# Optimization experiments

Hardware: AMD Instinct MI355X
Metric: run time of the kernel (lower is better)

The kernel has to match this reference:

```python
import jax, jax.numpy as jnp
import numpy as np

D_MODEL = 2048
H_TOTAL = 32
D_HEAD = D_MODEL // H_TOTAL  # 64
H_ACTIVE = 4
ROPE_BASE = 10000.0


def _apply_rope(t, cos, sin):
    # t: [B, H, T, DH]; cos/sin: [T, DH//2]; interleaved pair rotation
    t1 = t[..., 0::2]
    t2 = t[..., 1::2]
    r1 = t1 * cos - t2 * sin
    r2 = t1 * sin + t2 * cos
    return jnp.stack([r1, r2], axis=-1).reshape(t.shape)


def setup_inputs() -> dict:
    key = jax.random.key(0)
    ks = jax.random.split(key, 4)
    x = jax.random.normal(ks[0], (4, 1024, D_MODEL), dtype=jnp.float32)
    w_router = jax.random.normal(ks[1], (D_MODEL, H_TOTAL), dtype=jnp.float32) * 0.02
    w_qkv = jax.random.normal(ks[2], (D_MODEL, 3 * D_MODEL), dtype=jnp.float32) * 0.02
    w_out = jax.random.normal(ks[3], (D_MODEL, D_MODEL), dtype=jnp.float32) * 0.02
    return {"x": x, "w_router": w_router, "w_qkv": w_qkv, "w_out": w_out}


def reference(x, w_router, w_qkv, w_out):
    B, T, _ = x.shape
    # --- SwitchRouter: per-token probabilities over heads ---
    probs = jax.nn.softmax(x @ w_router, axis=-1)            # [B, T, H]
    # top-h_active heads per token (dense-math equivalent of sparse dispatch)
    _, top_idx = jax.lax.top_k(probs, H_ACTIVE)              # [B, T, HA]
    mask = jnp.sum(jax.nn.one_hot(top_idx, H_TOTAL, dtype=x.dtype), axis=-2)  # [B, T, H]
    gate = probs * mask                                      # router-scored gate

    # --- QKV projection ---
    qkv = x @ w_qkv                                          # [B, T, 3D]
    q, k, v = jnp.split(qkv, 3, axis=-1)
    def to_heads(t):
        return t.reshape(B, T, H_TOTAL, D_HEAD).transpose(0, 2, 1, 3)  # [B, H, T, DH]
    q, k, v = to_heads(q), to_heads(k), to_heads(v)

    # --- RoPE ---
    inv_freq = 1.0 / (ROPE_BASE ** (jnp.arange(0, D_HEAD, 2, dtype=jnp.float32) / D_HEAD))
    ang = jnp.arange(T, dtype=jnp.float32)[:, None] * inv_freq[None, :]  # [T, DH/2]
    cos, sin = jnp.cos(ang), jnp.sin(ang)
    q = _apply_rope(q, cos, sin)
    k = _apply_rope(k, cos, sin)

    # --- causal SDPA ---
    scores = jnp.einsum('bhqd,bhkd->bhqk', q, k) / np.float32(np.sqrt(D_HEAD))
    causal = jnp.tril(jnp.ones((T, T), dtype=bool))
    scores = jnp.where(causal, scores, jnp.finfo(scores.dtype).min)
    attn = jax.nn.softmax(scores, axis=-1)
    out = jnp.einsum('bhqk,bhkd->bhqd', attn, v)             # [B, H, T, DH]

    # --- gate: only active heads contribute (scatter-back equivalent) ---
    out = out * gate.transpose(0, 2, 1)[..., None]           # [B, H, T, DH]
    out = out.transpose(0, 2, 1, 3).reshape(B, T, D_MODEL)
    return out @ w_out
```

## Files before the change

### kernel.cpp

```cpp
#include <hip/hip_runtime.h>
#include <hip/hip_bf16.h>
#include <stdint.h>
#include <stddef.h>

typedef __attribute__((ext_vector_type(8))) short bf16x8;
typedef __attribute__((ext_vector_type(8))) unsigned short u16x8;
typedef __attribute__((ext_vector_type(4))) float f32x4;
typedef __attribute__((ext_vector_type(16))) float f32x16;

#define TT 1024

__device__ __forceinline__ unsigned short f2bf(float f){
  unsigned u = __builtin_bit_cast(unsigned, f);
  unsigned r = 0x7fffu + ((u >> 16) & 1u);
  return (unsigned short)((u + r) >> 16);
}
__device__ __forceinline__ float bf2f(unsigned short s){
  unsigned u = ((unsigned)s) << 16;
  return __builtin_bit_cast(float, u);
}
__device__ __forceinline__ void gload16(const unsigned short* g, unsigned short* l){
  __builtin_amdgcn_global_load_lds(
      (const __attribute__((address_space(1))) void*)g,
      (__attribute__((address_space(3))) void*)l, 16, 0, 0);
}

#define MFMA32(a, b, c) __builtin_amdgcn_mfma_f32_32x32x16_bf16((a), (b), (c), 0, 0, 0)
#define MFMA_B16(a, b, c) __builtin_amdgcn_mfma_f32_16x16x32_bf16((a), (b), (c), 0, 0, 0)

__global__ void transpose_cast_kernel(const float* __restrict__ in, unsigned short* __restrict__ out,
                                      int R, int C){
  __shared__ float tile[32][33];
  int c0 = blockIdx.x * 32, r0 = blockIdx.y * 32;
  for (int i = threadIdx.y; i < 32; i += 8)
    tile[i][threadIdx.x] = in[(size_t)(r0 + i) * C + c0 + threadIdx.x];
  __syncthreads();
  for (int i = threadIdx.y; i < 32; i += 8)
    out[(size_t)(c0 + i) * R + r0 + threadIdx.x] = f2bf(tile[threadIdx.x][i]);
}

__global__ void rope_table_kernel(float* __restrict__ tab){
  int idx = blockIdx.x * 256 + threadIdx.x;
  int pos = idx >> 5, i = idx & 31;
  float freq = powf(10000.0f, -(float)i / 32.0f);
  float ang = (float)pos * freq;
  tab[idx * 2]     = cosf(ang);
  tab[idx * 2 + 1] = sinf(ang);
}

__global__ __launch_bounds__(256) void prep_kernel(const float* __restrict__ x,
                                                   const float* __restrict__ wr,
                                                   unsigned short* __restrict__ x_bf,
                                                   float* __restrict__ gate,
                                                   unsigned char* __restrict__ heads4){
  __shared__ float xc[8 * 256];
  __shared__ float red[8 * 8 * 32];
  const int tid = threadIdx.x;
  const int tok0 = blockIdx.x * 8;
  const int p = tid >> 5, h = tid & 31;
  float acc[8] = {0.f,0.f,0.f,0.f,0.f,0.f,0.f,0.f};

  for (int kb = 0; kb < 8; kb++){
    __syncthreads();
    {
      int tok = tid >> 5, e = (tid & 31) * 8;
      const float* xp = x + (size_t)(tok0 + tok) * 2048 + kb * 256 + e;
      float4 v0 = *(const float4*)xp, v1 = *(const float4*)(xp + 4);
      float vals[8] = {v0.x, v0.y, v0.z, v0.w, v1.x, v1.y, v1.z, v1.w};
      u16x8 ob;
      #pragma unroll
      for (int jj = 0; jj < 8; jj++) ob[jj] = f2bf(vals[jj]);
      *(u16x8*)(x_bf + (size_t)(tok0 + tok) * 2048 + kb * 256 + e) = ob;
      #pragma unroll
      for (int jj = 0; jj < 8; jj++) xc[tok * 256 + e + jj] = vals[jj];
    }
    __syncthreads();
    const float* wp = wr + (size_t)(kb * 256 + p * 32) * 32 + h;
    #pragma unroll 4
    for (int j = 0; j < 32; j++){
      float wv = wp[j * 32];
      #pragma unroll
      for (int tok = 0; tok < 8; tok++)
        acc[tok] += xc[tok * 256 + p * 32 + j] * wv;
    }
  }
  #pragma unroll
  for (int tok = 0; tok < 8; tok++) red[(p * 8 + tok) * 32 + h] = acc[tok];
  __syncthreads();
  {
    int lane = tid & 63;
    int tok = (tid >> 6) * 2 + (lane >> 5);
    int hh = lane & 31;
    float logit = 0.f;
    #pragma unroll
    for (int pp = 0; pp < 8; pp++) logit += red[(pp * 8 + tok) * 32 + hh];
    float m = logit;
    #pragma unroll
    for (int s = 16; s >= 1; s >>= 1) m = fmaxf(m, __shfl_xor(m, s));
    float e = __expf(logit - m);
    float sum = e;
    #pragma unroll
    for (int s = 16; s >= 1; s >>= 1) sum += __shfl_xor(sum, s);
    float prob = e / sum;
    float v = logit; int sel = 0;
    #pragma unroll
    for (int rr2 = 0; rr2 < 4; rr2++){
      float bv = v; int bi = hh;
      #pragma unroll
      for (int s = 16; s >= 1; s >>= 1){
        float ov = __shfl_xor(bv, s); int oi = __shfl_xor(bi, s);
        if (ov > bv || (ov == bv && oi < bi)) { bv = ov; bi = oi; }
      }
      if (hh == bi) { sel = 1; v = -3.4e38f; }
    }
    gate[(size_t)(tok0 + tok) * 32 + hh] = sel ? prob : 0.f;
    unsigned long long bal = __ballot(sel != 0);
    unsigned selmask = (unsigned)(bal >> ((lane >> 5) * 32));
    if (sel){
      int r = __popc(selmask & ((1u << hh) - 1u));
      heads4[(size_t)(tok0 + tok) * 4 + r] = (unsigned char)hh;
    }
  }
}

__global__ void compact_kernel(const unsigned char* __restrict__ heads4,
                               unsigned short* __restrict__ idx, int* __restrict__ counts){
  int bh = blockIdx.x;
  int b = bh >> 5, h = bh & 31;
  int lane = threadIdx.x;
  int base = 0;
  for (int c = 0; c < 16; c++){
    int t = c * 64 + lane;
    unsigned u = ((const unsigned*)heads4)[b * 1024 + t];
    int r = -1;
    if (((u      ) & 255) == (unsigned)h) r = 0;
    else if (((u >>  8) & 255) == (unsigned)h) r = 1;
    else if (((u >> 16) & 255) == (unsigned)h) r = 2;
    else if (((u >> 24) & 255) == (unsigned)h) r = 3;
    bool act = (r >= 0);
    unsigned long long mask = __ballot(act);
    int pos = base + __popcll(mask & ((1ull << lane) - 1ull));
    if (act) idx[bh * 1024 + pos] = (unsigned short)(t | (r << 10));
    base += __popcll(mask);
  }
  if (lane == 0) counts[bh] = base;
}

__global__ __launch_bounds__(256) void qgemm_kernel(const unsigned short* __restrict__ x_bf,
                                                    const unsigned short* __restrict__ wqkvT,
                                                    const unsigned short* __restrict__ idx,
                                                    const int* __restrict__ counts,
                                                    const float* __restrict__ tab,
                                                    unsigned short* __restrict__ qact){
  __shared__ float red[4][64][64];
  const int bh = blockIdx.x, qt = blockIdx.y;
  const int count = counts[bh];
  if (qt * 64 >= count) return;
  const int b = bh >> 5, h = bh & 31;
  const int tid = threadIdx.x, lane = tid & 63, w = tid >> 6;
  const int li = lane & 15, lg = lane >> 4;
  const int nvalid = min(64, count - qt * 64);
  const unsigned short* myidx = idx + bh * 1024 + qt * 64;

  int atok[4];
  #pragma unroll
  for (int ai = 0; ai < 4; ai++){
    int s = ai * 16 + li;
    atok[ai] = (s < nvalid) ? (myidx[s] & 1023) : 0;
  }
  const unsigned short* Bbase = wqkvT + (size_t)(h * 64) * 2048;

  f32x4 acc[4][4];
  #pragma unroll
  for (int i = 0; i < 4; i++)
    #pragma unroll
    for (int j = 0; j < 4; j++) acc[i][j] = f32x4{0.f, 0.f, 0.f, 0.f};

  const int k0w = w * 512;
  #pragma unroll 2
  for (int ks = 0; ks < 16; ks++){
    int k0 = k0w + ks * 32 + lg * 8;
    bf16x8 af[4], bw[4];
    #pragma unroll
    for (int ai = 0; ai < 4; ai++)
      af[ai] = *(const bf16x8*)(x_bf + (size_t)(b * 1024 + atok[ai]) * 2048 + k0);
    #pragma unroll
    for (int ni = 0; ni < 4; ni++)
      bw[ni] = *(const bf16x8*)(Bbase + (size_t)(ni * 16 + li) * 2048 + k0);
    #pragma unroll
    for (int ai = 0; ai < 4; ai++)
      #pragma unroll
      for (int ni = 0; ni < 4; ni++)
        acc[ai][ni] = MFMA_B16(af[ai], bw[ni], acc[ai][ni]);
  }
  #pragma unroll
  for (int ai = 0; ai < 4; ai++)
    #pragma unroll
    for (int ni = 0; ni < 4; ni++)
      #pragma unroll
      for (int rr = 0; rr < 4; rr++)
        red[w][ai * 16 + lg * 4 + rr][ni * 16 + li] = acc[ai][ni][rr];
  __syncthreads();

  int q = tid >> 2, dbase = (tid & 3) * 16;
  if (q < nvalid){
    int e = myidx[q];
    int tok = e & 1023, r = e >> 10;
    unsigned short* op = qact + ((size_t)((b << 10) + tok) * 4 + r) * 64;
    const float* tp = tab + ((size_t)tok * 32 + (dbase >> 1)) * 2;
    #pragma unroll
    for (int p = 0; p < 8; p++){
      int d0 = dbase + 2 * p;
      float v0 = red[0][q][d0] + red[1][q][d0] + red[2][q][d0] + red[3][q][d0];
      float v1 = red[0][q][d0 + 1] + red[1][q][d0 + 1] + red[2][q][d0 + 1] + red[3][q][d0 + 1];
      float c = tp[2 * p], s = tp[2 * p + 1];
      op[d0]     = f2bf(v0 * c - v1 * s);
      op[d0 + 1] = f2bf(v0 * s + v1 * c);
    }
  }
}

template<int EPI>
__global__ __launch_bounds__(256, 1) void gemm32(const unsigned short* __restrict__ A,
                                                 const unsigned short* __restrict__ Bt,
                                                 float* __restrict__ Cf,
                                                 unsigned short* __restrict__ kbuf,
                                                 unsigned short* __restrict__ vt,
                                                 const float* __restrict__ tab,
                                                 int N, int K, int nbm){
  extern __shared__ unsigned short smem[];
  const int nblk = gridDim.x;
  const int raw = blockIdx.x;
  const int tile = (raw & 7) * (nblk >> 3) + (raw >> 3);
  const int bn = tile / nbm, bm = tile % nbm;

  const int tid = threadIdx.x, lane = tid & 63, wid = tid >> 6;
  const int wrow = wid >> 1, wcol = wid & 1;
  const int l31 = lane & 31, hi = lane >> 5;
  const int X = (l31 & 7) << 4;

  const unsigned short* gA[8];
  const unsigned short* gB[4];
  #pragma unroll
  for (int p = 0; p < 8; p++){
    int L = tid * 16 + p * 4096;
    int r = L >> 7, c = (L & 127) ^ ((r & 7) << 4);
    gA[p] = A + (size_t)(bm * 256 + r) * K + (c >> 1);
  }
  #pragma unroll
  for (int p = 0; p < 4; p++){
    int L = tid * 16 + p * 4096;
    int r = L >> 7, c = (L & 127) ^ ((r & 7) << 4);
    gB[p] = Bt + (size_t)(bn * 128 + r) * K + (c >> 1);
  }

  auto stageA0 = [&](int tt){
    unsigned short* b = smem + (tt % 3) * 24576;
    size_t ko = (size_t)tt * 64;
    gload16(gA[0] + ko, b + tid * 8);
    gload16(gA[1] + ko, b + tid * 8 + 2048);
    gload16(gA[2] + ko, b + tid * 8 + 4096);
    gload16(gA[3] + ko, b + tid * 8 + 6144);
  };
  auto stageA1 = [&](int tt){
    unsigned short* b = smem + (tt % 3) * 24576;
    size_t ko = (size_t)tt * 64;
    gload16(gA[4] + ko, b + tid * 8 + 8192);
    gload16(gA[5] + ko, b + tid * 8 + 10240);
    gload16(gA[6] + ko, b + tid * 8 + 12288);
    gload16(gA[7] + ko, b + tid * 8 + 14336);
  };
  auto stageB = [&](int tt){
    unsigned short* b = smem + (tt % 3) * 24576 + 16384;
    size_t ko = (size_t)tt * 64;
    gload16(gB[0] + ko, b + tid * 8);
    gload16(gB[1] + ko, b + tid * 8 + 2048);
    gload16(gB[2] + ko, b + tid * 8 + 4096);
    gload16(gB[3] + ko, b + tid * 8 + 6144);
  };

  f32x16 acc[4][2];
  #pragma unroll
  for (int i = 0; i < 4; i++)
    #pragma unroll
    for (int j = 0; j < 2; j++) acc[i][j] = f32x16{0,0,0,0,0,0,0,0,0,0,0,0,0,0,0,0};

  const int NT = K >> 6;
  stageA0(0); stageA1(0); stageB(0);
  stageA0(1); stageA1(1); stageB(1);

  const int arow = (wrow * 128 + l31) * 64;
  const int brow = 16384 + (wcol * 64 + l31) * 64;

  for (int t = 0; t < NT; ++t){
    if (t < NT - 1) asm volatile("s_waitcnt vmcnt(12)" ::: "memory");
    else            asm volatile("s_waitcnt vmcnt(0)" ::: "memory");
    __builtin_amdgcn_s_barrier();
    __builtin_amdgcn_sched_barrier(0);
    const unsigned short* bs = smem + (t % 3) * 24576;
    const bool st = (t + 2 < NT);
    #pragma unroll
    for (int ks = 0; ks < 4; ks++){
      const int kp = ((ks * 32 + hi * 16) ^ X) >> 1;
      bf16x8 a0 = *(const bf16x8*)(bs + arow +        kp);
      bf16x8 a1 = *(const bf16x8*)(bs + arow + 2048 + kp);
      bf16x8 a2 = *(const bf16x8*)(bs + arow + 4096 + kp);
      bf16x8 a3 = *(const bf16x8*)(bs + arow + 6144 + kp);
      bf16x8 b0 = *(const bf16x8*)(bs + brow +        kp);
      bf16x8 b1 = *(const bf16x8*)(bs + brow + 2048 + kp);
      if (st && ks == 0) stageA0(t + 2);
      if (st && ks == 1) stageA1(t + 2);
      if (st && ks == 2) stageB(t + 2);
      acc[0][0] = MFMA32(a0, b0, acc[0][0]); acc[0][1] = MFMA32(a0, b1, acc[0][1]);
      acc[1][0] = MFMA32(a1, b0, acc[1][0]); acc[1][1] = MFMA32(a1, b1, acc[1][1]);
      acc[2][0] = MFMA32(a2, b0, acc[2][0]); acc[2][1] = MFMA32(a2, b1, acc[2][1]);
      acc[3][0] = MFMA32(a3, b0, acc[3][0]); acc[3][1] = MFMA32(a3, b1, acc[3][1]);
    }
  }

  if (EPI == 1){
    if (bn < 16){
      #pragma unroll
      for (int i = 0; i < 4; i++){
        #pragma unroll
        for (int j = 0; j < 2; j++){
          int col = bn * 128 + wcol * 64 + j * 32 + l31;
          int ii = (col & 63) >> 1;
          #pragma unroll
          for (int g = 0; g < 4; g++){
            #pragma unroll
            for (int rr = 0; rr < 4; rr++){
              int row = bm * 256 + wrow * 128 + i * 32 + g * 8 + hi * 4 + rr;
              int pos = row & (TT - 1);
              const float* tp = tab + ((size_t)pos * 32 + ii) * 2;
              float c = tp[0], s = tp[1];
              float val = acc[i][j][g * 4 + rr];
              float pv = __shfl_xor(val, 1);
              float res = (lane & 1) ? (pv * s + val * c) : (val * c - pv * s);
              kbuf[(size_t)row * 2048 + col] = f2bf(res);
            }
          }
        }
      }
    } else {
      #pragma unroll
      for (int i = 0; i < 4; i++){
        #pragma unroll
        for (int j = 0; j < 2; j++){
          int vcol = bn * 128 + wcol * 64 + j * 32 + l31 - 2048;
          int hh = vcol >> 6, d = vcol & 63;
          int row0 = bm * 256 + wrow * 128 + i * 32 + hi * 4;
          int b = row0 >> 10, t0 = row0 & (TT - 1);
          #pragma unroll
          for (int g = 0; g < 4; g++){
            ushort4 pk;
            pk.x = f2bf(acc[i][j][g * 4 + 0]); pk.y = f2bf(acc[i][j][g * 4 + 1]);
            pk.z = f2bf(acc[i][j][g * 4 + 2]); pk.w = f2bf(acc[i][j][g * 4 + 3]);
            *(ushort4*)(vt + ((size_t)((b * 32 + hh) * 64 + d)) * TT + t0 + g * 8) = pk;
          }
        }
      }
    }
  } else {
    #pragma unroll
    for (int i = 0; i < 4; i++){
      #pragma unroll
      for (int j = 0; j < 2; j++){
        int col = bn * 128 + wcol * 64 + j * 32 + l31;
        #pragma unroll
        for (int g = 0; g < 4; g++){
          #pragma unroll
          for (int rr = 0; rr < 4; rr++){
            size_t row = (size_t)(bm * 256 + wrow * 128 + i * 32 + g * 8 + hi * 4 + rr);
            Cf[row * N + col] = acc[i][j][g * 4 + rr];
          }
        }
      }
    }
  }
}

__global__ __launch_bounds__(256) void attn_sparse_kernel(const unsigned short* __restrict__ qact,
                                                          const unsigned short* __restrict__ kbuf,
                                                          const unsigned short* __restrict__ vt,
                                                          const float* __restrict__ gate,
                                                          const unsigned short* __restrict__ idx,
                                                          const int* __restrict__ counts,
                                                          unsigned short* __restrict__ attn_out){
  __shared__ unsigned short Ks[64 * 64];
  __shared__ unsigned short Vs[64 * 64];
  __shared__ unsigned short Ps[4][16 * 64];
  const int bh = blockIdx.x, qt = blockIdx.y;
  const int count = counts[bh];
  if (qt * 64 >= count) return;
  const int b = bh >> 5, h = bh & 31;
  const int tid = threadIdx.x, lane = tid & 63, w = tid >> 6;
  const int li = lane & 15, lg = lane >> 4;
  const unsigned short* myidx = idx + bh * 1024 + qt * 64;
  const int nvalid = min(64, count - qt * 64);
  const int qmax = myidx[nvalid - 1] & 1023;

  int qi[4];
  #pragma unroll
  for (int r = 0; r < 4; r++){
    int s = w * 16 + lg * 4 + r;
    qi[r] = (s < nvalid) ? (myidx[s] & 1023) : -1;
  }
  bf16x8 qf0, qf1;
  {
    int s = w * 16 + li;
    int e2 = (s < nvalid) ? myidx[s] : 0;
    const unsigned short* qp = qact + ((size_t)((b << 10) + (e2 & 1023)) * 4 + (e2 >> 10)) * 64;
    qf0 = *(const bf16x8*)(qp + lg * 8);
    qf1 = *(const bf16x8*)(qp + 32 + lg * 8);
  }
  f32x4 o[4];
  #pragma unroll
  for (int i = 0; i < 4; i++) o[i] = f32x4{0.f, 0.f, 0.f, 0.f};
  float m_run[4], l_run[4];
  #pragma unroll
  for (int r = 0; r < 4; r++){ m_run[r] = -1e30f; l_run[r] = 0.f; }

  const int nkt = (qmax >> 6) + 1;
  for (int kt = 0; kt < nkt; kt++){
    const int kb = kt * 64;
    #pragma unroll
    for (int s2 = 0; s2 < 2; s2++){
      int s = s2 * 256 + tid;
      int r = s >> 3, c = (s & 7) * 8;
      gload16(kbuf + (size_t)(b * TT + kb + r) * 2048 + h * 64 + c, &Ks[s * 8]);
      gload16(vt + (size_t)(bh * 64 + r) * TT + kb + c, &Vs[s * 8]);
    }
    __syncthreads();

    f32x4 s4[4];
    #pragma unroll
    for (int ni = 0; ni < 4; ni++){
      bf16x8 k0 = *(const bf16x8*)(&Ks[(ni * 16 + li) * 64 + lg * 8]);
      bf16x8 k1 = *(const bf16x8*)(&Ks[(ni * 16 + li) * 64 + 32 + lg * 8]);
      f32x4 t = f32x4{0.f, 0.f, 0.f, 0.f};
      t = MFMA_B16(qf0, k0, t);
      t = MFMA_B16(qf1, k1, t);
      s4[ni] = t;
    }
    float mt[4];
    #pragma unroll
    for (int r = 0; r < 4; r++) mt[r] = -1e30f;
    #pragma unroll
    for (int ni = 0; ni < 4; ni++){
      int kidx = kb + ni * 16 + li;
      #pragma unroll
      for (int r = 0; r < 4; r++){
        float val = s4[ni][r] * 0.125f;
        val = (kidx <= qi[r]) ? val : -1e30f;
        s4[ni][r] = val;
        mt[r] = fmaxf(mt[r], val);
      }
    }
    #pragma unroll
    for (int r = 0; r < 4; r++){
      #pragma unroll
      for (int sh = 8; sh >= 1; sh >>= 1) mt[r] = fmaxf(mt[r], __shfl_xor(mt[r], sh));
      float mnew = fmaxf(m_run[r], mt[r]);
      float corr = __expf(m_run[r] - mnew);
      m_run[r] = mnew;
      l_run[r] *= corr;
      #pragma unroll
      for (int j = 0; j < 4; j++) o[j][r] *= corr;
    }
    float rs[4] = {0.f, 0.f, 0.f, 0.f};
    #pragma unroll
    for (int ni = 0; ni < 4; ni++)
      #pragma unroll
      for (int r = 0; r < 4; r++){
        float p = __expf(s4[ni][r] - m_run[r]);
        s4[ni][r] = p;
        rs[r] += p;
      }
    #pragma unroll
    for (int r = 0; r < 4; r++){
      #pragma unroll
      for (int sh = 8; sh >= 1; sh >>= 1) rs[r] += __shfl_xor(rs[r], sh);
      l_run[r] += rs[r];
    }
    #pragma unroll
    for (int ni = 0; ni < 4; ni++)
      #pragma unroll
      for (int r = 0; r < 4; r++)
        Ps[w][(lg * 4 + r) * 64 + ni * 16 + li] = f2bf(s4[ni][r]);
    #pragma unroll
    for (int ks = 0; ks < 2; ks++){
      bf16x8 pa = *(const bf16x8*)(&Ps[w][li * 64 + ks * 32 + lg * 8]);
      #pragma unroll
      for (int ni = 0; ni < 4; ni++){
        bf16x8 vb = *(const bf16x8*)(&Vs[(ni * 16 + li) * 64 + ks * 32 + lg * 8]);
        o[ni] = MFMA_B16(pa, vb, o[ni]);
      }
    }
    __syncthreads();
  }
  #pragma unroll
  for (int r = 0; r < 4; r++){
    if (qi[r] < 0) continue;
    float g = gate[(size_t)(b * TT + qi[r]) * 32 + h];
    float inv = g / l_run[r];
    #pragma unroll
    for (int ni = 0; ni < 4; ni++)
      attn_out[(size_t)(b * TT + qi[r]) * 2048 + h * 64 + ni * 16 + li] = f2bf(o[ni][r] * inv);
  }
}

extern "C" void kernel_launch(void* const* d_in, const int* in_sizes, int n_in,
                              void* d_out, int out_size, void* d_ws, size_t ws_size,
                              hipStream_t stream){
  const float* x        = (const float*)d_in[0];
  const float* w_router = (const float*)d_in[1];
  const float* w_qkv    = (const float*)d_in[2];
  const float* w_out    = (const float*)d_in[3];
  float* out = (float*)d_out;
  char* ws = (char*)d_ws;

  unsigned short* kbuf   = (unsigned short*)(ws);
  unsigned short* vt     = (unsigned short*)(ws + 16777216);
  unsigned short* qact   = (unsigned short*)(ws + 33554432);
  unsigned short* idx    = (unsigned short*)(ws + 37748736);
  int* counts            = (int*)(ws + 38010880);
  unsigned char* heads4  = (unsigned char*)(ws + 38011392);
  unsigned short* x_bf   = (unsigned short*)(ws + 50331648);
  unsigned short* wqkvT  = (unsigned short*)(ws + 67108864);
  unsigned short* woutT  = (unsigned short*)(ws + 92274688);
  float* gate            = (float*)(ws + 100663296);
  float* tab             = (float*)(ws + 101187584);
  unsigned short* attn   = x_bf;

  constexpr int GEMM_LDS = 147456;
  (void)hipFuncSetAttribute(reinterpret_cast<const void*>(&gemm32<1>),
                            hipFuncAttributeMaxDynamicSharedMemorySize, GEMM_LDS);
  (void)hipFuncSetAttribute(reinterpret_cast<const void*>(&gemm32<0>),
                            hipFuncAttributeMaxDynamicSharedMemorySize, GEMM_LDS);

  hipLaunchKernelGGL(transpose_cast_kernel, dim3(192, 64), dim3(32, 8), 0, stream, w_qkv, wqkvT, 2048, 6144);
  hipLaunchKernelGGL(transpose_cast_kernel, dim3(64, 64), dim3(32, 8), 0, stream, w_out, woutT, 2048, 2048);
  hipLaunchKernelGGL(rope_table_kernel, dim3(128), dim3(256), 0, stream, tab);
  hipLaunchKernelGGL(prep_kernel, dim3(512), dim3(256), 0, stream, x, w_router, x_bf, gate, heads4);
  hipLaunchKernelGGL(compact_kernel, dim3(128), dim3(64), 0, stream, heads4, idx, counts);
  hipLaunchKernelGGL((gemm32<1>), dim3(512), dim3(256), GEMM_LDS, stream,
                     x_bf, wqkvT + (size_t)2048 * 2048, (float*)nullptr, kbuf, vt, tab, 4096, 2048, 16);
  hipLaunchKernelGGL(qgemm_kernel, dim3(128, 16), dim3(256), 0, stream,
                     x_bf, wqkvT, idx, counts, tab, qact);
  (void)hipMemsetAsync(attn, 0, (size_t)4096 * 2048 * 2, stream);
  hipLaunchKernelGGL(attn_sparse_kernel, dim3(128, 16), dim3(256), 0, stream,
                     qact, kbuf, vt, gate, idx, counts, attn);
  hipLaunchKernelGGL((gemm32<0>), dim3(256), dim3(256), GEMM_LDS, stream,
                     attn, woutT, out, (unsigned short*)nullptr, (unsigned short*)nullptr,
                     (const float*)nullptr, 2048, 2048, 16);
}
```

Measured before the change: 263.5 us.

## Fuse Q projection into attention, retile GEMMs, merge prep kernels, swizzle LDS

```diff
diff --git a/kernel.cpp b/kernel.cpp
--- a/kernel.cpp
+++ b/kernel.cpp
@@ -28,10 +28,15 @@
 #define MFMA32(a, b, c) __builtin_amdgcn_mfma_f32_32x32x16_bf16((a), (b), (c), 0, 0, 0)
 #define MFMA_B16(a, b, c) __builtin_amdgcn_mfma_f32_16x16x32_bf16((a), (b), (c), 0, 0, 0)
 
-__global__ void transpose_cast_kernel(const float* __restrict__ in, unsigned short* __restrict__ out,
-                                      int R, int C){
+__global__ void transpose_w_kernel(const float* __restrict__ wqkv, const float* __restrict__ wout,
+                                   unsigned short* __restrict__ wqkvT, unsigned short* __restrict__ woutT){
   __shared__ float tile[32][33];
-  int c0 = blockIdx.x * 32, r0 = blockIdx.y * 32;
+  const float* in; unsigned short* out; int C;
+  int bx = blockIdx.x;
+  if (bx < 192){ in = wqkv; out = wqkvT; C = 6144; }
+  else         { in = wout; out = woutT; C = 2048; bx -= 192; }
+  const int R = 2048;
+  int c0 = bx * 32, r0 = blockIdx.y * 32;
   for (int i = threadIdx.y; i < 32; i += 8)
     tile[i][threadIdx.x] = in[(size_t)(r0 + i) * C + c0 + threadIdx.x];
   __syncthreads();
@@ -39,27 +44,28 @@
     out[(size_t)(c0 + i) * R + r0 + threadIdx.x] = f2bf(tile[threadIdx.x][i]);
 }
 
-__global__ void rope_table_kernel(float* __restrict__ tab){
-  int idx = blockIdx.x * 256 + threadIdx.x;
-  int pos = idx >> 5, i = idx & 31;
-  float freq = powf(10000.0f, -(float)i / 32.0f);
-  float ang = (float)pos * freq;
-  tab[idx * 2]     = cosf(ang);
-  tab[idx * 2 + 1] = sinf(ang);
-}
-
 __global__ __launch_bounds__(256) void prep_kernel(const float* __restrict__ x,
                                                    const float* __restrict__ wr,
                                                    unsigned short* __restrict__ x_bf,
                                                    float* __restrict__ gate,
-                                                   unsigned char* __restrict__ heads4){
+                                                   unsigned char* __restrict__ heads4,
+                                                   float* __restrict__ tab){
   __shared__ float xc[8 * 256];
   __shared__ float red[8 * 8 * 32];
   const int tid = threadIdx.x;
   const int tok0 = blockIdx.x * 8;
   const int p = tid >> 5, h = tid & 31;
+
+  if (blockIdx.x < 128){
+    int i2 = blockIdx.x * 256 + tid;
+    int pos = i2 >> 5, ii = i2 & 31;
+    float freq = powf(10000.0f, -(float)ii / 32.0f);
+    float ang = (float)pos * freq;
+    tab[i2 * 2]     = cosf(ang);
+    tab[i2 * 2 + 1] = sinf(ang);
+  }
+
   float acc[8] = {0.f,0.f,0.f,0.f,0.f,0.f,0.f,0.f};
-
   for (int kb = 0; kb < 8; kb++){
     __syncthreads();
     {
@@ -146,89 +152,18 @@
   if (lane == 0) counts[bh] = base;
 }
 
-__global__ __launch_bounds__(256) void qgemm_kernel(const unsigned short* __restrict__ x_bf,
-                                                    const unsigned short* __restrict__ wqkvT,
-                                                    const unsigned short* __restrict__ idx,
-                                                    const int* __restrict__ counts,
-                                                    const float* __restrict__ tab,
-                                                    unsigned short* __restrict__ qact){
-  __shared__ float red[4][64][64];
-  const int bh = blockIdx.x, qt = blockIdx.y;
-  const int count = counts[bh];
-  if (qt * 64 >= count) return;
-  const int b = bh >> 5, h = bh & 31;
-  const int tid = threadIdx.x, lane = tid & 63, w = tid >> 6;
-  const int li = lane & 15, lg = lane >> 4;
-  const int nvalid = min(64, count - qt * 64);
-  const unsigned short* myidx = idx + bh * 1024 + qt * 64;
-
-  int atok[4];
-  #pragma unroll
-  for (int ai = 0; ai < 4; ai++){
-    int s = ai * 16 + li;
-    atok[ai] = (s < nvalid) ? (myidx[s] & 1023) : 0;
-  }
-  const unsigned short* Bbase = wqkvT + (size_t)(h * 64) * 2048;
-
-  f32x4 acc[4][4];
-  #pragma unroll
-  for (int i = 0; i < 4; i++)
-    #pragma unroll
-    for (int j = 0; j < 4; j++) acc[i][j] = f32x4{0.f, 0.f, 0.f, 0.f};
-
-  const int k0w = w * 512;
-  #pragma unroll 2
-  for (int ks = 0; ks < 16; ks++){
-    int k0 = k0w + ks * 32 + lg * 8;
-    bf16x8 af[4], bw[4];
-    #pragma unroll
-    for (int ai = 0; ai < 4; ai++)
-      af[ai] = *(const bf16x8*)(x_bf + (size_t)(b * 1024 + atok[ai]) * 2048 + k0);
-    #pragma unroll
-    for (int ni = 0; ni < 4; ni++)
-      bw[ni] = *(const bf16x8*)(Bbase + (size_t)(ni * 16 + li) * 2048 + k0);
-    #pragma unroll
-    for (int ai = 0; ai < 4; ai++)
-      #pragma unroll
-      for (int ni = 0; ni < 4; ni++)
-        acc[ai][ni] = MFMA_B16(af[ai], bw[ni], acc[ai][ni]);
-  }
-  #pragma unroll
-  for (int ai = 0; ai < 4; ai++)
-    #pragma unroll
-    for (int ni = 0; ni < 4; ni++)
-      #pragma unroll
-      for (int rr = 0; rr < 4; rr++)
-        red[w][ai * 16 + lg * 4 + rr][ni * 16 + li] = acc[ai][ni][rr];
-  __syncthreads();
-
-  int q = tid >> 2, dbase = (tid & 3) * 16;
-  if (q < nvalid){
-    int e = myidx[q];
-    int tok = e & 1023, r = e >> 10;
-    unsigned short* op = qact + ((size_t)((b << 10) + tok) * 4 + r) * 64;
-    const float* tp = tab + ((size_t)tok * 32 + (dbase >> 1)) * 2;
-    #pragma unroll
-    for (int p = 0; p < 8; p++){
-      int d0 = dbase + 2 * p;
-      float v0 = red[0][q][d0] + red[1][q][d0] + red[2][q][d0] + red[3][q][d0];
-      float v1 = red[0][q][d0 + 1] + red[1][q][d0 + 1] + red[2][q][d0 + 1] + red[3][q][d0 + 1];
-      float c = tp[2 * p], s = tp[2 * p + 1];
-      op[d0]     = f2bf(v0 * c - v1 * s);
-      op[d0 + 1] = f2bf(v0 * s + v1 * c);
-    }
-  }
-}
-
-template<int EPI>
-__global__ __launch_bounds__(256, 1) void gemm32(const unsigned short* __restrict__ A,
-                                                 const unsigned short* __restrict__ Bt,
-                                                 float* __restrict__ Cf,
-                                                 unsigned short* __restrict__ kbuf,
-                                                 unsigned short* __restrict__ vt,
-                                                 const float* __restrict__ tab,
-                                                 int N, int K, int nbm){
+template<int MREP, int EPI>
+__global__ __launch_bounds__(256, 2) void gemmk(const unsigned short* __restrict__ A,
+                                                const unsigned short* __restrict__ Bt,
+                                                float* __restrict__ Cf,
+                                                unsigned short* __restrict__ kbuf,
+                                                unsigned short* __restrict__ vt,
+                                                const float* __restrict__ tab,
+                                                int N, int K, int nbm){
   extern __shared__ unsigned short smem[];
+  constexpr int BM = MREP * 64;
+  constexpr int AU = MREP * 2048;
+  constexpr int SLOT = AU + 4096;
   const int nblk = gridDim.x;
   const int raw = blockIdx.x;
   const int tile = (raw & 7) * (nblk >> 3) + (raw >> 3);
@@ -237,91 +172,87 @@
   const int tid = threadIdx.x, lane = tid & 63, wid = tid >> 6;
   const int wrow = wid >> 1, wcol = wid & 1;
   const int l31 = lane & 31, hi = lane >> 5;
-  const int X = (l31 & 7) << 4;
-
-  const unsigned short* gA[8];
-  const unsigned short* gB[4];
-  #pragma unroll
-  for (int p = 0; p < 8; p++){
+  const int X = ((l31 >> 1) & 7) << 4;
+
+  const unsigned short* gA[MREP];
+  const unsigned short* gB[2];
+  #pragma unroll
+  for (int p = 0; p < MREP; p++){
     int L = tid * 16 + p * 4096;
-    int r = L >> 7, c = (L & 127) ^ ((r & 7) << 4);
-    gA[p] = A + (size_t)(bm * 256 + r) * K + (c >> 1);
-  }
-  #pragma unroll
-  for (int p = 0; p < 4; p++){
+    int line = L >> 7;
+    int cs = (L & 127) ^ ((line & 7) << 4);
+    gA[p] = A + (size_t)(bm * BM + line * 2 + (cs >> 6)) * K + ((cs & 63) >> 1);
+  }
+  #pragma unroll
+  for (int p = 0; p < 2; p++){
     int L = tid * 16 + p * 4096;
-    int r = L >> 7, c = (L & 127) ^ ((r & 7) << 4);
-    gB[p] = Bt + (size_t)(bn * 128 + r) * K + (c >> 1);
-  }
-
-  auto stageA0 = [&](int tt){
-    unsigned short* b = smem + (tt % 3) * 24576;
-    size_t ko = (size_t)tt * 64;
-    gload16(gA[0] + ko, b + tid * 8);
-    gload16(gA[1] + ko, b + tid * 8 + 2048);
-    gload16(gA[2] + ko, b + tid * 8 + 4096);
-    gload16(gA[3] + ko, b + tid * 8 + 6144);
-  };
-  auto stageA1 = [&](int tt){
-    unsigned short* b = smem + (tt % 3) * 24576;
-    size_t ko = (size_t)tt * 64;
-    gload16(gA[4] + ko, b + tid * 8 + 8192);
-    gload16(gA[5] + ko, b + tid * 8 + 10240);
-    gload16(gA[6] + ko, b + tid * 8 + 12288);
-    gload16(gA[7] + ko, b + tid * 8 + 14336);
-  };
-  auto stageB = [&](int tt){
-    unsigned short* b = smem + (tt % 3) * 24576 + 16384;
-    size_t ko = (size_t)tt * 64;
-    gload16(gB[0] + ko, b + tid * 8);
-    gload16(gB[1] + ko, b + tid * 8 + 2048);
-    gload16(gB[2] + ko, b + tid * 8 + 4096);
-    gload16(gB[3] + ko, b + tid * 8 + 6144);
-  };
-
-  f32x16 acc[4][2];
-  #pragma unroll
-  for (int i = 0; i < 4; i++)
+    int line = L >> 7;
+    int cs = (L & 127) ^ ((line & 7) << 4);
+    gB[p] = Bt + (size_t)(bn * 128 + line * 2 + (cs >> 6)) * K + ((cs & 63) >> 1);
+  }
+
+  f32x16 acc[MREP][2];
+  #pragma unroll
+  for (int i = 0; i < MREP; i++)
     #pragma unroll
     for (int j = 0; j < 2; j++) acc[i][j] = f32x16{0,0,0,0,0,0,0,0,0,0,0,0,0,0,0,0};
 
-  const int NT = K >> 6;
-  stageA0(0); stageA1(0); stageB(0);
-  stageA0(1); stageA1(1); stageB(1);
-
-  const int arow = (wrow * 128 + l31) * 64;
-  const int brow = 16384 + (wcol * 64 + l31) * 64;
+  const int NT = K >> 5;
+  #pragma unroll
+  for (int tt = 0; tt < 2; tt++){
+    unsigned short* sb = smem + tt * SLOT;
+    #pragma unroll
+    for (int p = 0; p < MREP; p++) gload16(gA[p] + (size_t)tt * 32, sb + tid * 8 + p * 2048);
+    #pragma unroll
+    for (int p = 0; p < 2; p++)    gload16(gB[p] + (size_t)tt * 32, sb + AU + tid * 8 + p * 2048);
+  }
 
   for (int t = 0; t < NT; ++t){
-    if (t < NT - 1) asm volatile("s_waitcnt vmcnt(12)" ::: "memory");
-    else            asm volatile("s_waitcnt vmcnt(0)" ::: "memory");
+    if (t < NT - 1){
+      if constexpr (MREP == 4) asm volatile("s_waitcnt vmcnt(6)" ::: "memory");
+      else                     asm volatile("s_waitcnt vmcnt(4)" ::: "memory");
+    } else                     asm volatile("s_waitcnt vmcnt(0)" ::: "memory");
     __builtin_amdgcn_s_barrier();
     __builtin_amdgcn_sched_barrier(0);
-    const unsigned short* bs = smem + (t % 3) * 24576;
+    const unsigned short* bs = smem + (t % 3) * SLOT;
+    unsigned short* ns = smem + ((t + 2) % 3) * SLOT;
     const bool st = (t + 2 < NT);
     #pragma unroll
-    for (int ks = 0; ks < 4; ks++){
-      const int kp = ((ks * 32 + hi * 16) ^ X) >> 1;
-      bf16x8 a0 = *(const bf16x8*)(bs + arow +        kp);
-      bf16x8 a1 = *(const bf16x8*)(bs + arow + 2048 + kp);
-      bf16x8 a2 = *(const bf16x8*)(bs + arow + 4096 + kp);
-      bf16x8 a3 = *(const bf16x8*)(bs + arow + 6144 + kp);
-      bf16x8 b0 = *(const bf16x8*)(bs + brow +        kp);
-      bf16x8 b1 = *(const bf16x8*)(bs + brow + 2048 + kp);
-      if (st && ks == 0) stageA0(t + 2);
-      if (st && ks == 1) stageA1(t + 2);
-      if (st && ks == 2) stageB(t + 2);
-      acc[0][0] = MFMA32(a0, b0, acc[0][0]); acc[0][1] = MFMA32(a0, b1, acc[0][1]);
-      acc[1][0] = MFMA32(a1, b0, acc[1][0]); acc[1][1] = MFMA32(a1, b1, acc[1][1]);
-      acc[2][0] = MFMA32(a2, b0, acc[2][0]); acc[2][1] = MFMA32(a2, b1, acc[2][1]);
-      acc[3][0] = MFMA32(a3, b0, acc[3][0]); acc[3][1] = MFMA32(a3, b1, acc[3][1]);
-    }
-  }
-
-  if (EPI == 1){
+    for (int ks = 0; ks < 2; ks++){
+      const int bo = (((l31 & 1) * 64 + ks * 32 + hi * 16) ^ X) >> 1;
+      bf16x8 av[MREP], bv[2];
+      #pragma unroll
+      for (int i = 0; i < MREP; i++)
+        av[i] = *(const bf16x8*)(bs + (wrow * (MREP * 16) + i * 16 + (l31 >> 1)) * 64 + bo);
+      #pragma unroll
+      for (int j = 0; j < 2; j++)
+        bv[j] = *(const bf16x8*)(bs + AU + (wcol * 32 + j * 16 + (l31 >> 1)) * 64 + bo);
+      if (st){
+        if (ks == 0){
+          #pragma unroll
+          for (int p = 0; p < MREP / 2 + 1; p++)
+            gload16(gA[p] + (size_t)(t + 2) * 32, ns + tid * 8 + p * 2048);
+        } else {
+          #pragma unroll
+          for (int p = MREP / 2 + 1; p < MREP; p++)
+            gload16(gA[p] + (size_t)(t + 2) * 32, ns + tid * 8 + p * 2048);
+          #pragma unroll
+          for (int p = 0; p < 2; p++)
+            gload16(gB[p] + (size_t)(t + 2) * 32, ns + AU + tid * 8 + p * 2048);
+        }
+      }
+      #pragma unroll
+      for (int i = 0; i < MREP; i++){
+        acc[i][0] = MFMA32(av[i], bv[0], acc[i][0]);
+        acc[i][1] = MFMA32(av[i], bv[1], acc[i][1]);
+      }
+    }
+  }
+
+  if constexpr (EPI == 1){
     if (bn < 16){
       #pragma unroll
-      for (int i = 0; i < 4; i++){
+      for (int i = 0; i < MREP; i++){
         #pragma unroll
         for (int j = 0; j < 2; j++){
           int col = bn * 128 + wcol * 64 + j * 32 + l31;
@@ -330,7 +261,7 @@
           for (int g = 0; g < 4; g++){
             #pragma unroll
             for (int rr = 0; rr < 4; rr++){
-              int row = bm * 256 + wrow * 128 + i * 32 + g * 8 + hi * 4 + rr;
+              int row = bm * BM + wrow * (BM / 2) + i * 32 + g * 8 + hi * 4 + rr;
               int pos = row & (TT - 1);
               const float* tp = tab + ((size_t)pos * 32 + ii) * 2;
               float c = tp[0], s = tp[1];
@@ -344,12 +275,12 @@
       }
     } else {
       #pragma unroll
-      for (int i = 0; i < 4; i++){
+      for (int i = 0; i < MREP; i++){
         #pragma unroll
         for (int j = 0; j < 2; j++){
           int vcol = bn * 128 + wcol * 64 + j * 32 + l31 - 2048;
           int hh = vcol >> 6, d = vcol & 63;
-          int row0 = bm * 256 + wrow * 128 + i * 32 + hi * 4;
+          int row0 = bm * BM + wrow * (BM / 2) + i * 32 + hi * 4;
           int b = row0 >> 10, t0 = row0 & (TT - 1);
           #pragma unroll
           for (int g = 0; g < 4; g++){
@@ -363,7 +294,7 @@
     }
   } else {
     #pragma unroll
-    for (int i = 0; i < 4; i++){
+    for (int i = 0; i < MREP; i++){
       #pragma unroll
       for (int j = 0; j < 2; j++){
         int col = bn * 128 + wcol * 64 + j * 32 + l31;
@@ -371,7 +302,7 @@
         for (int g = 0; g < 4; g++){
           #pragma unroll
           for (int rr = 0; rr < 4; rr++){
-            size_t row = (size_t)(bm * 256 + wrow * 128 + i * 32 + g * 8 + hi * 4 + rr);
+            size_t row = (size_t)(bm * BM + wrow * (BM / 2) + i * 32 + g * 8 + hi * 4 + rr);
             Cf[row * N + col] = acc[i][j][g * 4 + rr];
           }
         }
@@ -380,16 +311,19 @@
   }
 }
 
-__global__ __launch_bounds__(256) void attn_sparse_kernel(const unsigned short* __restrict__ qact,
-                                                          const unsigned short* __restrict__ kbuf,
-                                                          const unsigned short* __restrict__ vt,
-                                                          const float* __restrict__ gate,
-                                                          const unsigned short* __restrict__ idx,
-                                                          const int* __restrict__ counts,
-                                                          unsigned short* __restrict__ attn_out){
+__global__ __launch_bounds__(256) void attn_fused(const unsigned short* __restrict__ x_bf,
+                                                  const unsigned short* __restrict__ wqkvT,
+                                                  const unsigned short* __restrict__ kbuf,
+                                                  const unsigned short* __restrict__ vt,
+                                                  const float* __restrict__ gate,
+                                                  const unsigned short* __restrict__ idx,
+                                                  const int* __restrict__ counts,
+                                                  const float* __restrict__ tab,
+                                                  unsigned short* __restrict__ attn_out){
   __shared__ unsigned short Ks[64 * 64];
   __shared__ unsigned short Vs[64 * 64];
   __shared__ unsigned short Ps[4][16 * 64];
+  __shared__ unsigned short Qb[4][16 * 64];
   const int bh = blockIdx.x, qt = blockIdx.y;
   const int count = counts[bh];
   if (qt * 64 >= count) return;
@@ -406,14 +340,45 @@
     int s = w * 16 + lg * 4 + r;
     qi[r] = (s < nvalid) ? (myidx[s] & 1023) : -1;
   }
-  bf16x8 qf0, qf1;
+
   {
     int s = w * 16 + li;
-    int e2 = (s < nvalid) ? myidx[s] : 0;
-    const unsigned short* qp = qact + ((size_t)((b << 10) + (e2 & 1023)) * 4 + (e2 >> 10)) * 64;
-    qf0 = *(const bf16x8*)(qp + lg * 8);
-    qf1 = *(const bf16x8*)(qp + 32 + lg * 8);
-  }
+    int tokA = (s < nvalid) ? (myidx[s] & 1023) : 0;
+    const unsigned short* xrow = x_bf + (size_t)(b * 1024 + tokA) * 2048;
+    const unsigned short* wq = wqkvT + (size_t)(h * 64) * 2048;
+    f32x4 qa[4];
+    #pragma unroll
+    for (int ni = 0; ni < 4; ni++) qa[ni] = f32x4{0.f, 0.f, 0.f, 0.f};
+    #pragma unroll 2
+    for (int kk = 0; kk < 64; kk++){
+      int k0 = kk * 32 + lg * 8;
+      bf16x8 af = *(const bf16x8*)(xrow + k0);
+      #pragma unroll
+      for (int ni = 0; ni < 4; ni++){
+        bf16x8 bw = *(const bf16x8*)(wq + (size_t)(ni * 16 + li) * 2048 + k0);
+        qa[ni] = MFMA_B16(af, bw, qa[ni]);
+      }
+    }
+    #pragma unroll
+    for (int ni = 0; ni < 4; ni++){
+      int col = ni * 16 + li;
+      #pragma unroll
+      for (int r = 0; r < 4; r++){
+        int tq = (qi[r] < 0) ? 0 : qi[r];
+        const float* tp = tab + ((size_t)tq * 32 + (col >> 1)) * 2;
+        float c = tp[0], sn = tp[1];
+        float val = qa[ni][r];
+        float pv = __shfl_xor(val, 1);
+        float res = (li & 1) ? (pv * sn + val * c) : (val * c - pv * sn);
+        int row = lg * 4 + r;
+        Qb[w][(row * 128 + ((col * 2) ^ ((row & 7) << 4))) >> 1] = f2bf(res * 0.125f);
+      }
+    }
+  }
+  const int kX = (li & 7) << 4;
+  bf16x8 qf0 = *(const bf16x8*)(&Qb[w][(li * 128 + ((lg * 16) ^ kX)) >> 1]);
+  bf16x8 qf1 = *(const bf16x8*)(&Qb[w][(li * 128 + ((64 + lg * 16) ^ kX)) >> 1]);
+
   f32x4 o[4];
   #pragma unroll
   for (int i = 0; i < 4; i++) o[i] = f32x4{0.f, 0.f, 0.f, 0.f};
@@ -426,18 +391,20 @@
     const int kb = kt * 64;
     #pragma unroll
     for (int s2 = 0; s2 < 2; s2++){
-      int s = s2 * 256 + tid;
-      int r = s >> 3, c = (s & 7) * 8;
-      gload16(kbuf + (size_t)(b * TT + kb + r) * 2048 + h * 64 + c, &Ks[s * 8]);
-      gload16(vt + (size_t)(bh * 64 + r) * TT + kb + c, &Vs[s * 8]);
+      int ss = s2 * 256 + tid;
+      int r = ss >> 3;
+      int ce = (((ss & 7) * 16) ^ ((r & 7) << 4)) >> 1;
+      gload16(kbuf + (size_t)(b * TT + kb + r) * 2048 + h * 64 + ce, &Ks[ss * 8]);
+      gload16(vt + (size_t)(bh * 64 + r) * TT + kb + ce, &Vs[ss * 8]);
     }
     __syncthreads();
 
     f32x4 s4[4];
     #pragma unroll
     for (int ni = 0; ni < 4; ni++){
-      bf16x8 k0 = *(const bf16x8*)(&Ks[(ni * 16 + li) * 64 + lg * 8]);
-      bf16x8 k1 = *(const bf16x8*)(&Ks[(ni * 16 + li) * 64 + 32 + lg * 8]);
+      int rb = (ni * 16 + li) * 128;
+      bf16x8 k0 = *(const bf16x8*)(&Ks[(rb + ((lg * 16) ^ kX)) >> 1]);
+      bf16x8 k1 = *(const bf16x8*)(&Ks[(rb + ((64 + lg * 16) ^ kX)) >> 1]);
       f32x4 t = f32x4{0.f, 0.f, 0.f, 0.f};
       t = MFMA_B16(qf0, k0, t);
       t = MFMA_B16(qf1, k1, t);
@@ -451,7 +418,7 @@
       int kidx = kb + ni * 16 + li;
       #pragma unroll
       for (int r = 0; r < 4; r++){
-        float val = s4[ni][r] * 0.125f;
+        float val = s4[ni][r];
         val = (kidx <= qi[r]) ? val : -1e30f;
         s4[ni][r] = val;
         mt[r] = fmaxf(mt[r], val);
@@ -486,14 +453,16 @@
     #pragma unroll
     for (int ni = 0; ni < 4; ni++)
       #pragma unroll
-      for (int r = 0; r < 4; r++)
-        Ps[w][(lg * 4 + r) * 64 + ni * 16 + li] = f2bf(s4[ni][r]);
+      for (int r = 0; r < 4; r++){
+        int row = lg * 4 + r;
+        Ps[w][(row * 128 + (((ni * 16 + li) * 2) ^ ((row & 7) << 4))) >> 1] = f2bf(s4[ni][r]);
+      }
     #pragma unroll
     for (int ks = 0; ks < 2; ks++){
-      bf16x8 pa = *(const bf16x8*)(&Ps[w][li * 64 + ks * 32 + lg * 8]);
+      bf16x8 pa = *(const bf16x8*)(&Ps[w][(li * 128 + ((ks * 64 + lg * 16) ^ kX)) >> 1]);
       #pragma unroll
       for (int ni = 0; ni < 4; ni++){
-        bf16x8 vb = *(const bf16x8*)(&Vs[(ni * 16 + li) * 64 + ks * 32 + lg * 8]);
+        bf16x8 vb = *(const bf16x8*)(&Vs[((ni * 16 + li) * 128 + ((ks * 64 + lg * 16) ^ kX)) >> 1]);
         o[ni] = MFMA_B16(pa, vb, o[ni]);
       }
     }
@@ -522,7 +491,6 @@
 
   unsigned short* kbuf   = (unsigned short*)(ws);
   unsigned short* vt     = (unsigned short*)(ws + 16777216);
-  unsigned short* qact   = (unsigned short*)(ws + 33554432);
   unsigned short* idx    = (unsigned short*)(ws + 37748736);
   int* counts            = (int*)(ws + 38010880);
   unsigned char* heads4  = (unsigned char*)(ws + 38011392);
@@ -531,27 +499,24 @@
   unsigned short* woutT  = (unsigned short*)(ws + 92274688);
   float* gate            = (float*)(ws + 100663296);
   float* tab             = (float*)(ws + 101187584);
-  unsigned short* attn   = x_bf;
-
-  constexpr int GEMM_LDS = 147456;
-  (void)hipFuncSetAttribute(reinterpret_cast<const void*>(&gemm32<1>),
-                            hipFuncAttributeMaxDynamicSharedMemorySize, GEMM_LDS);
-  (void)hipFuncSetAttribute(reinterpret_cast<const void*>(&gemm32<0>),
-                            hipFuncAttributeMaxDynamicSharedMemorySize, GEMM_LDS);
-
-  hipLaunchKernelGGL(transpose_cast_kernel, dim3(192, 64), dim3(32, 8), 0, stream, w_qkv, wqkvT, 2048, 6144);
-  hipLaunchKernelGGL(transpose_cast_kernel, dim3(64, 64), dim3(32, 8), 0, stream, w_out, woutT, 2048, 2048);
-  hipLaunchKernelGGL(rope_table_kernel, dim3(128), dim3(256), 0, stream, tab);
-  hipLaunchKernelGGL(prep_kernel, dim3(512), dim3(256), 0, stream, x, w_router, x_bf, gate, heads4);
+  unsigned short* attn   = (unsigned short*)(ws + 67108864 + 8388608);
+
+  constexpr int KV_LDS  = 3 * (4 * 4096 + 8192);
+  constexpr int OUT_LDS = 3 * (2 * 4096 + 8192);
+  (void)hipFuncSetAttribute(reinterpret_cast<const void*>(&gemmk<4, 1>),
+                            hipFuncAttributeMaxDynamicSharedMemorySize, KV_LDS);
+  (void)hipFuncSetAttribute(reinterpret_cast<const void*>(&gemmk<2, 0>),
+                            hipFuncAttributeMaxDynamicSharedMemorySize, OUT_LDS);
+
+  hipLaunchKernelGGL(transpose_w_kernel, dim3(256, 64), dim3(32, 8), 0, stream, w_qkv, w_out, wqkvT, woutT);
+  hipLaunchKernelGGL(prep_kernel, dim3(512), dim3(256), 0, stream, x, w_router, x_bf, gate, heads4, tab);
   hipLaunchKernelGGL(compact_kernel, dim3(128), dim3(64), 0, stream, heads4, idx, counts);
-  hipLaunchKernelGGL((gemm32<1>), dim3(512), dim3(256), GEMM_LDS, stream,
+  hipLaunchKernelGGL((gemmk<4, 1>), dim3(512), dim3(256), KV_LDS, stream,
                      x_bf, wqkvT + (size_t)2048 * 2048, (float*)nullptr, kbuf, vt, tab, 4096, 2048, 16);
-  hipLaunchKernelGGL(qgemm_kernel, dim3(128, 16), dim3(256), 0, stream,
-                     x_bf, wqkvT, idx, counts, tab, qact);
   (void)hipMemsetAsync(attn, 0, (size_t)4096 * 2048 * 2, stream);
-  hipLaunchKernelGGL(attn_sparse_kernel, dim3(128, 16), dim3(256), 0, stream,
-                     qact, kbuf, vt, gate, idx, counts, attn);
-  hipLaunchKernelGGL((gemm32<0>), dim3(256), dim3(256), GEMM_LDS, stream,
+  hipLaunchKernelGGL(attn_fused, dim3(128, 16), dim3(256), 0, stream,
+                     x_bf, wqkvT, kbuf, vt, gate, idx, counts, tab, attn);
+  hipLaunchKernelGGL((gemmk<2, 0>), dim3(512), dim3(256), OUT_LDS, stream,
                      attn, woutT, out, (unsigned short*)nullptr, (unsigned short*)nullptr,
-                     (const float*)nullptr, 2048, 2048, 16);
-}
+                     (const float*)nullptr, 2048, 2048, 32);
+}
```

Measured after the change: 297.8 us. 13.0% more time.
